# Kernel tuning notes

Measured on AMD Instinct MI355X. Metric: run time of the kernel, lower is better.

The kernel has to match this reference:

```python
import jax, jax.numpy as jnp
import numpy as np
from jax import lax

K = 7          # kernel size
G = 12         # groups
EPS = 1e-5


def bn(x, gamma, beta, axes):
    # training-mode batch norm (torch default train() mode uses batch stats)
    mean = jnp.mean(x, axis=axes, keepdims=True)
    var = jnp.var(x, axis=axes, keepdims=True)
    shape = [1] * x.ndim
    shape[1 if x.ndim == 4 else -1] = -1
    g = gamma.reshape(shape)
    b = beta.reshape(shape)
    return g * (x - mean) * lax.rsqrt(var + EPS) + b


def setup_inputs() -> dict:
    key = jax.random.key(0)
    ks = jax.random.split(key, 12)
    B, C, H, Wd = 16, 192, 32, 32
    Cr = C // 4                      # reduce_mapping out channels = out_channels // reduce_ratio = 48
    flat = C * H * Wd                # 196608
    inp = {
        "x": jax.random.normal(ks[0], (B, C, H, Wd), jnp.float32),
        "Wr": jax.random.normal(ks[1], (Cr, C), jnp.float32) * 0.05,          # reduce_mapping 1x1 conv
        "gamma_s": jnp.ones((Cr,), jnp.float32),
        "beta_s": jnp.zeros((Cr,), jnp.float32),
        "Ws": jax.random.normal(ks[2], (K * K * G, Cr), jnp.float32) * 0.05,  # span_mapping 1x1 conv
        "W1": jax.random.normal(ks[3], (512, flat), jnp.float32) * 0.002,
        "b1": jnp.zeros((512,), jnp.float32),
        "g1": jnp.ones((512,), jnp.float32),
        "beta1": jnp.zeros((512,), jnp.float32),
        "W2": jax.random.normal(ks[4], (128, 512), jnp.float32) * 0.04,
        "b2": jnp.zeros((128,), jnp.float32),
        "g2": jnp.ones((128,), jnp.float32),
        "beta2": jnp.zeros((128,), jnp.float32),
        "W3": jax.random.normal(ks[5], (17, 128), jnp.float32) * 0.09,
        "b3": jnp.zeros((17,), jnp.float32),
    }
    return inp


def reference(x, Wr, gamma_s, beta_s, Ws, W1, b1, g1, beta1, W2, b2, g2, beta2, W3, b3):
    B, C, H, Wd = x.shape
    Cg = C // G
    # unfold (im2col) with kernel 7, pad 3, stride 1, dil 1 -> [B, C*K*K, H, W]
    # channel ordering (c, kh, kw) matches torch.nn.Unfold
    patches = lax.conv_general_dilated_patches(x, (K, K), (1, 1), [(K // 2, K // 2)] * 2)
    unf = patches.reshape(B, G, Cg, K * K, H, Wd)
    # kernel generation path: 1x1 reduce conv -> BN+ReLU -> 1x1 span conv
    red = jnp.einsum('bchw,oc->bohw', x, Wr)
    red = jax.nn.relu(bn(red, gamma_s, beta_s, (0, 2, 3)))
    ker = jnp.einsum('bchw,oc->bohw', red, Ws).reshape(B, G, K * K, H, Wd)
    # involution: per-pixel kernel multiply + sum over K*K
    out = jnp.einsum('bgkhw,bgckhw->bgchw', ker, unf).reshape(B, C, H, Wd)
    # classifier head
    flat = out.reshape(B, -1)
    h = jax.nn.relu(bn(flat @ W1.T + b1, g1, beta1, (0,)))
    h = jax.nn.relu(bn(h @ W2.T + b2, g2, beta2, (0,)))
    return h @ W3.T + b3
```

## Files before the change

### kernel.cpp

```cpp
#include <hip/hip_runtime.h>

#define EPS 1e-5f

typedef float v4f __attribute__((ext_vector_type(4)));

__global__ __launch_bounds__(256) void k_reduce_conv(
    const float* __restrict__ x, const float* __restrict__ Wr,
    float* __restrict__ red, float* __restrict__ spart)
{
  int ob = blockIdx.x >> 6;
  int pb = blockIdx.x & 63;
  int o0 = ob * 6;
  int pix = (pb << 8) + threadIdx.x;
  int b = pix >> 10;
  int hw = pix & 1023;
  const float* xp = x + ((size_t)b * 192) * 1024 + hw;
  float acc[6] = {0.f, 0.f, 0.f, 0.f, 0.f, 0.f};
  for (int c = 0; c < 192; ++c) {
    float xv = xp[(size_t)c * 1024];
#pragma unroll
    for (int j = 0; j < 6; ++j)
      acc[j] = fmaf(xv, Wr[(o0 + j) * 192 + c], acc[j]);
  }
#pragma unroll
  for (int j = 0; j < 6; ++j)
    red[(size_t)(o0 + j) * 16384 + pix] = acc[j];

  int t = threadIdx.x, lane = t & 63, wid = t >> 6;
  float sv[6], qv[6];
#pragma unroll
  for (int j = 0; j < 6; ++j) { sv[j] = acc[j]; qv[j] = acc[j] * acc[j]; }
#pragma unroll
  for (int off = 32; off > 0; off >>= 1)
#pragma unroll
    for (int j = 0; j < 6; ++j) {
      sv[j] += __shfl_down(sv[j], off);
      qv[j] += __shfl_down(qv[j], off);
    }
  __shared__ float ps[4][12];
  if (lane == 0)
#pragma unroll
    for (int j = 0; j < 6; ++j) { ps[wid][j] = sv[j]; ps[wid][6 + j] = qv[j]; }
  __syncthreads();
  if (t < 12) {
    float v = ps[0][t] + ps[1][t] + ps[2][t] + ps[3][t];
    int j = t % 6, s = t / 6;
    spart[(size_t)(s * 48 + o0 + j) * 64 + pb] = v;
  }
}

__global__ __launch_bounds__(128) void k_stats2(
    const float* __restrict__ spart, float* __restrict__ stats)
{
  int t = threadIdx.x;
  if (t < 96) {
    const v4f* p = (const v4f*)(spart + (size_t)t * 64);
    v4f s = p[0];
#pragma unroll
    for (int i = 1; i < 16; ++i) s += p[i];
    stats[t] = s.x + s.y + s.z + s.w;
  }
}

__global__ __launch_bounds__(256) void k_invol(
    const float* __restrict__ x, const float* __restrict__ red,
    const float* __restrict__ stats, const float* __restrict__ gamma_s,
    const float* __restrict__ beta_s, const float* __restrict__ Ws,
    float* __restrict__ flat)
{
  __shared__ __align__(16) float xt[196 * 20];
  __shared__ __align__(16) float redn[64 * 52];
  __shared__ __align__(16) float kt[49 * 64];

  int bx = blockIdx.x;
  int tile = bx & 15;
  int g = (bx >> 4) % 12;
  int b = bx / 192;
  int th = (tile >> 2) * 8, tw = (tile & 3) * 8;
  int t = threadIdx.x;

  for (int idx = t; idx < 16 * 196; idx += 256) {
    int c = idx / 196, s = idx - c * 196;
    int r = s / 14, q = s - r * 14;
    int sh = th + r - 3, sw = tw + q - 3;
    float v = 0.f;
    if (sh >= 0 && sh < 32 && sw >= 0 && sw < 32)
      v = x[(((size_t)b * 192 + g * 16 + c) << 10) + (sh << 5) + sw];
    xt[s * 20 + c] = v;
  }
  for (int idx = t; idx < 64 * 48; idx += 256) {
    int p = idx & 63, o = idx >> 6;
    int py = p >> 3, px = p & 7;
    float mean = stats[o] * (1.f / 16384.f);
    float var = fmaf(-mean, mean, stats[48 + o] * (1.f / 16384.f));
    float sc = gamma_s[o] * rsqrtf(var + EPS);
    float sh_ = fmaf(-mean, sc, beta_s[o]);
    float v = red[(size_t)o * 16384 + (b << 10) + ((th + py) << 5) + (tw + px)];
    redn[p * 52 + o] = fmaxf(fmaf(v, sc, sh_), 0.f);
  }
  __syncthreads();

  {
    int p = t & 63;
    int kg = __builtin_amdgcn_readfirstlane(t >> 6);
    int k0 = kg * 13;
    float acc[13];
#pragma unroll
    for (int j = 0; j < 13; ++j) acc[j] = 0.f;
    const float* wsp = Ws + (size_t)(g * 49 + k0) * 48;
    for (int o4 = 0; o4 < 48; o4 += 4) {
      v4f rv = *(const v4f*)&redn[p * 52 + o4];
#pragma unroll
      for (int j = 0; j < 13; ++j)
        if (k0 + j < 49) {
          acc[j] = fmaf(rv.x, wsp[j * 48 + o4 + 0], acc[j]);
          acc[j] = fmaf(rv.y, wsp[j * 48 + o4 + 1], acc[j]);
          acc[j] = fmaf(rv.z, wsp[j * 48 + o4 + 2], acc[j]);
          acc[j] = fmaf(rv.w, wsp[j * 48 + o4 + 3], acc[j]);
        }
    }
#pragma unroll
    for (int j = 0; j < 13; ++j)
      if (k0 + j < 49) kt[(k0 + j) * 64 + p] = acc[j];
  }
  __syncthreads();

  {
    int p = t & 63, cq = t >> 6;
    int c0 = cq * 4;
    int py = p >> 3, px = p & 7;
    float a0 = 0.f, a1 = 0.f, a2 = 0.f, a3 = 0.f;
#pragma unroll
    for (int k = 0; k < 49; ++k) {
      int dh = k / 7, dw = k - dh * 7;
      float kv = kt[k * 64 + p];
      const v4f xv = *(const v4f*)&xt[((py + dh) * 14 + px + dw) * 20 + c0];
      a0 = fmaf(kv, xv.x, a0);
      a1 = fmaf(kv, xv.y, a1);
      a2 = fmaf(kv, xv.z, a2);
      a3 = fmaf(kv, xv.w, a3);
    }
    size_t base = (((size_t)b * 192 + g * 16 + c0) << 10) + ((th + py) << 5) + (tw + px);
    flat[base] = a0;
    flat[base + 1024] = a1;
    flat[base + 2048] = a2;
    flat[base + 3072] = a3;
  }
}

__global__ __launch_bounds__(256) void k_gemm1(
    const float* __restrict__ flat, const float* __restrict__ W1,
    float* __restrict__ h1part)
{
  int kc = blockIdx.x;
  int n0 = blockIdx.y * 8;
  int t = threadIdx.x;
  int kt = t & 127;
  int bg = t >> 7;
  int b0 = bg * 8;

  const v4f* W1v = (const v4f*)W1;
  const v4f* flatv = (const v4f*)flat;

  float acc[8][8];
#pragma unroll
  for (int n = 0; n < 8; ++n)
#pragma unroll
    for (int j = 0; j < 8; ++j) acc[n][j] = 0.f;

  int kv = kc * 6144 + kt;

  v4f w[8], wn[8], f[8];
#pragma unroll
  for (int n = 0; n < 8; ++n)
    w[n] = W1v[(size_t)(n0 + n) * 49152 + kv];

#define GEMM1_PHASE(CUR, NXT, PRE)                                         \
  {                                                                        \
    _Pragma("unroll")                                                      \
    for (int j = 0; j < 8; ++j)                                            \
      f[j] = flatv[(size_t)(b0 + j) * 49152 + kv];                         \
    if (PRE) {                                                             \
      _Pragma("unroll")                                                    \
      for (int n = 0; n < 8; ++n)                                          \
        NXT[n] = W1v[(size_t)(n0 + n) * 49152 + kv + 128];                 \
    }                                                                      \
    _Pragma("unroll")                                                      \
    for (int j = 0; j < 8; ++j)                                            \
      _Pragma("unroll")                                                    \
      for (int n = 0; n < 8; ++n) {                                        \
        acc[n][j] = fmaf(CUR[n].x, f[j].x, acc[n][j]);                     \
        acc[n][j] = fmaf(CUR[n].y, f[j].y, acc[n][j]);                     \
        acc[n][j] = fmaf(CUR[n].z, f[j].z, acc[n][j]);                     \
        acc[n][j] = fmaf(CUR[n].w, f[j].w, acc[n][j]);                     \
      }                                                                    \
    kv += 128;                                                             \
  }

#pragma unroll 1
  for (int it = 0; it < 24; ++it) {
    GEMM1_PHASE(w, wn, true)
    GEMM1_PHASE(wn, w, (it < 23))
  }
#undef GEMM1_PHASE

  __shared__ float rbuf[256 * 33];
#pragma unroll
  for (int pass = 0; pass < 2; ++pass) {
    __syncthreads();
#pragma unroll
    for (int nn = 0; nn < 4; ++nn)
#pragma unroll
      for (int j = 0; j < 8; ++j)
        rbuf[t * 33 + nn * 8 + j] = acc[pass * 4 + nn][j];
    __syncthreads();
    int v = t >> 2;
    int c = v & 31, bgsel = v >> 5;
    int i = t & 3;
    float s = 0.f;
#pragma unroll
    for (int r = 0; r < 32; ++r)
      s += rbuf[(bgsel * 128 + i + (r << 2)) * 33 + c];
    s += __shfl_down(s, 2, 4);
    s += __shfl_down(s, 1, 4);
    if (i == 0) {
      int nn = c >> 3, j = c & 7;
      int b = bgsel * 8 + j;
      h1part[(size_t)kc * 8192 + b * 512 + n0 + pass * 4 + nn] = s;
    }
  }
}

__global__ __launch_bounds__(256) void k_bn1(
    const float* __restrict__ h1part, const float* __restrict__ g1,
    const float* __restrict__ beta1, float* __restrict__ h1)
{
  int n = blockIdx.x * 256 + threadIdx.x;
  float v[16];
#pragma unroll
  for (int b = 0; b < 16; ++b) v[b] = 0.f;
#pragma unroll
  for (int y = 0; y < 8; ++y)
#pragma unroll
    for (int b = 0; b < 16; ++b)
      v[b] += h1part[(size_t)y * 8192 + b * 512 + n];
  float s = 0.f;
#pragma unroll
  for (int b = 0; b < 16; ++b) s += v[b];
  float mean = s * (1.f / 16.f);
  float q = 0.f;
#pragma unroll
  for (int b = 0; b < 16; ++b) { float d = v[b] - mean; q = fmaf(d, d, q); }
  float inv = rsqrtf(q * (1.f / 16.f) + EPS);
  float sc = g1[n] * inv, sh = beta1[n];
#pragma unroll
  for (int b = 0; b < 16; ++b)
    h1[b * 512 + n] = fmaxf(fmaf(v[b] - mean, sc, sh), 0.f);
}

__global__ __launch_bounds__(256) void k_gemm2(
    const float* __restrict__ h1, const float* __restrict__ W2,
    float* __restrict__ h2pre)
{
  int gid = blockIdx.x * 256 + threadIdx.x;
  int b = gid >> 7, m = gid & 127;
  const float* hp = h1 + b * 512;
  const float* wp = W2 + m * 512;
  float s = 0.f;
  for (int n = 0; n < 512; n += 4) {
    v4f hv = *(const v4f*)(hp + n);
    v4f wv = *(const v4f*)(wp + n);
    s = fmaf(hv.x, wv.x, s);
    s = fmaf(hv.y, wv.y, s);
    s = fmaf(hv.z, wv.z, s);
    s = fmaf(hv.w, wv.w, s);
  }
  h2pre[b * 128 + m] = s;
}

__global__ __launch_bounds__(320) void k_tail(
    const float* __restrict__ h2pre, const float* __restrict__ g2,
    const float* __restrict__ beta2, const float* __restrict__ W3,
    const float* __restrict__ b3, float* __restrict__ out)
{
  __shared__ float h2[16 * 128];
  int t = threadIdx.x;
  if (t < 128) {
    float v[16];
    float s = 0.f;
#pragma unroll
    for (int b = 0; b < 16; ++b) { v[b] = h2pre[b * 128 + t]; s += v[b]; }
    float mean = s * (1.f / 16.f);
    float q = 0.f;
#pragma unroll
    for (int b = 0; b < 16; ++b) { float d = v[b] - mean; q = fmaf(d, d, q); }
    float inv = rsqrtf(q * (1.f / 16.f) + EPS);
    float sc = g2[t] * inv, sh = beta2[t];
#pragma unroll
    for (int b = 0; b < 16; ++b)
      h2[b * 128 + t] = fmaxf(fmaf(v[b] - mean, sc, sh), 0.f);
  }
  __syncthreads();
  if (t < 272) {
    int b = t / 17, j = t - b * 17;
    float s = b3[j];
    const float* hp = h2 + b * 128;
    const float* wp = W3 + j * 128;
#pragma unroll 4
    for (int m = 0; m < 128; ++m) s = fmaf(hp[m], wp[m], s);
    out[t] = s;
  }
}

extern "C" void kernel_launch(void* const* d_in, const int* in_sizes, int n_in,
                              void* d_out, int out_size, void* d_ws, size_t ws_size,
                              hipStream_t stream)
{
  const float* x       = (const float*)d_in[0];
  const float* Wr      = (const float*)d_in[1];
  const float* gamma_s = (const float*)d_in[2];
  const float* beta_s  = (const float*)d_in[3];
  const float* Ws      = (const float*)d_in[4];
  const float* W1      = (const float*)d_in[5];
  const float* g1      = (const float*)d_in[7];
  const float* beta1   = (const float*)d_in[8];
  const float* W2      = (const float*)d_in[9];
  const float* g2      = (const float*)d_in[11];
  const float* beta2   = (const float*)d_in[12];
  const float* W3      = (const float*)d_in[13];
  const float* b3      = (const float*)d_in[14];

  float* ws = (float*)d_ws;
  float* red    = ws;
  float* flat   = red + 786432;
  float* stats  = flat + 3145728;
  float* spart  = stats + 96;
  float* h1part = spart + 6144;
  float* h1     = h1part + 65536;
  float* h2pre  = h1 + 8192;

  k_reduce_conv<<<512, 256, 0, stream>>>(x, Wr, red, spart);
  k_stats2<<<1, 128, 0, stream>>>(spart, stats);
  k_invol<<<3072, 256, 0, stream>>>(x, red, stats, gamma_s, beta_s, Ws, flat);
  k_gemm1<<<dim3(8, 64), 256, 0, stream>>>(flat, W1, h1part);
  k_bn1<<<2, 256, 0, stream>>>(h1part, g1, beta1, h1);
  k_gemm2<<<8, 256, 0, stream>>>(h1, W2, h2pre);
  k_tail<<<1, 320, 0, stream>>>(h2pre, g2, beta2, W3, b3, (float*)d_out);
}
```

Before: 302.3 us.

## Fuse stats into involution, re-tile gemm1, fuse BN1 into gemm2

Removes the single-block stats kernel and has every involution block recompute the BN statistics from the partial sums in shared memory. The big W1 GEMM is re-tiled to 4 outputs per block with half the K-chunk, giving a 16x128 grid (4x more blocks), fewer registers per thread and a launch-bounds occupancy hint. The BN1 kernel is folded into gemm2, so each block redundantly reduces the now-16 partial slices. This cuts two launches and raises parallelism in the dominant GEMM, at the cost of redundant stats work and a larger partial-sum buffer.

```diff
diff --git a/kernel.cpp b/kernel.cpp
--- a/kernel.cpp
+++ b/kernel.cpp
@@ -49,28 +49,16 @@
   }
 }
 
-__global__ __launch_bounds__(128) void k_stats2(
-    const float* __restrict__ spart, float* __restrict__ stats)
-{
-  int t = threadIdx.x;
-  if (t < 96) {
-    const v4f* p = (const v4f*)(spart + (size_t)t * 64);
-    v4f s = p[0];
-#pragma unroll
-    for (int i = 1; i < 16; ++i) s += p[i];
-    stats[t] = s.x + s.y + s.z + s.w;
-  }
-}
-
 __global__ __launch_bounds__(256) void k_invol(
     const float* __restrict__ x, const float* __restrict__ red,
-    const float* __restrict__ stats, const float* __restrict__ gamma_s,
+    const float* __restrict__ spart, const float* __restrict__ gamma_s,
     const float* __restrict__ beta_s, const float* __restrict__ Ws,
     float* __restrict__ flat)
 {
   __shared__ __align__(16) float xt[196 * 20];
   __shared__ __align__(16) float redn[64 * 52];
   __shared__ __align__(16) float kt[49 * 64];
+  __shared__ float sstats[96];
 
   int bx = blockIdx.x;
   int tile = bx & 15;
@@ -78,6 +66,14 @@
   int b = bx / 192;
   int th = (tile >> 2) * 8, tw = (tile & 3) * 8;
   int t = threadIdx.x;
+
+  if (t < 96) {
+    const v4f* p = (const v4f*)(spart + (size_t)t * 64);
+    v4f s4 = p[0];
+#pragma unroll
+    for (int i = 1; i < 16; ++i) s4 += p[i];
+    sstats[t] = s4.x + s4.y + s4.z + s4.w;
+  }
 
   for (int idx = t; idx < 16 * 196; idx += 256) {
     int c = idx / 196, s = idx - c * 196;
@@ -88,11 +84,13 @@
       v = x[(((size_t)b * 192 + g * 16 + c) << 10) + (sh << 5) + sw];
     xt[s * 20 + c] = v;
   }
+  __syncthreads();
+
   for (int idx = t; idx < 64 * 48; idx += 256) {
     int p = idx & 63, o = idx >> 6;
     int py = p >> 3, px = p & 7;
-    float mean = stats[o] * (1.f / 16384.f);
-    float var = fmaf(-mean, mean, stats[48 + o] * (1.f / 16384.f));
+    float mean = sstats[o] * (1.f / 16384.f);
+    float var = fmaf(-mean, mean, sstats[48 + o] * (1.f / 16384.f));
     float sc = gamma_s[o] * rsqrtf(var + EPS);
     float sh_ = fmaf(-mean, sc, beta_s[o]);
     float v = red[(size_t)o * 16384 + (b << 10) + ((th + py) << 5) + (tw + px)];
@@ -148,12 +146,12 @@
   }
 }
 
-__global__ __launch_bounds__(256) void k_gemm1(
+__global__ __launch_bounds__(256, 4) void k_gemm1(
     const float* __restrict__ flat, const float* __restrict__ W1,
     float* __restrict__ h1part)
 {
   int kc = blockIdx.x;
-  int n0 = blockIdx.y * 8;
+  int n0 = blockIdx.y * 4;
   int t = threadIdx.x;
   int kt = t & 127;
   int bg = t >> 7;
@@ -162,17 +160,17 @@
   const v4f* W1v = (const v4f*)W1;
   const v4f* flatv = (const v4f*)flat;
 
-  float acc[8][8];
-#pragma unroll
-  for (int n = 0; n < 8; ++n)
+  float acc[4][8];
+#pragma unroll
+  for (int n = 0; n < 4; ++n)
 #pragma unroll
     for (int j = 0; j < 8; ++j) acc[n][j] = 0.f;
 
-  int kv = kc * 6144 + kt;
-
-  v4f w[8], wn[8], f[8];
-#pragma unroll
-  for (int n = 0; n < 8; ++n)
+  int kv = kc * 3072 + kt;
+
+  v4f w[4], wn[4], f[8];
+#pragma unroll
+  for (int n = 0; n < 4; ++n)
     w[n] = W1v[(size_t)(n0 + n) * 49152 + kv];
 
 #define GEMM1_PHASE(CUR, NXT, PRE)                                         \
@@ -182,13 +180,13 @@
       f[j] = flatv[(size_t)(b0 + j) * 49152 + kv];                         \
     if (PRE) {                                                             \
       _Pragma("unroll")                                                    \
-      for (int n = 0; n < 8; ++n)                                          \
+      for (int n = 0; n < 4; ++n)                                          \
         NXT[n] = W1v[(size_t)(n0 + n) * 49152 + kv + 128];                 \
     }                                                                      \
     _Pragma("unroll")                                                      \
     for (int j = 0; j < 8; ++j)                                            \
       _Pragma("unroll")                                                    \
-      for (int n = 0; n < 8; ++n) {                                        \
+      for (int n = 0; n < 4; ++n) {                                        \
         acc[n][j] = fmaf(CUR[n].x, f[j].x, acc[n][j]);                     \
         acc[n][j] = fmaf(CUR[n].y, f[j].y, acc[n][j]);                     \
         acc[n][j] = fmaf(CUR[n].z, f[j].z, acc[n][j]);                     \
@@ -198,22 +196,20 @@
   }
 
 #pragma unroll 1
-  for (int it = 0; it < 24; ++it) {
+  for (int it = 0; it < 12; ++it) {
     GEMM1_PHASE(w, wn, true)
-    GEMM1_PHASE(wn, w, (it < 23))
+    GEMM1_PHASE(wn, w, (it < 11))
   }
 #undef GEMM1_PHASE
 
   __shared__ float rbuf[256 * 33];
 #pragma unroll
-  for (int pass = 0; pass < 2; ++pass) {
-    __syncthreads();
-#pragma unroll
-    for (int nn = 0; nn < 4; ++nn)
-#pragma unroll
-      for (int j = 0; j < 8; ++j)
-        rbuf[t * 33 + nn * 8 + j] = acc[pass * 4 + nn][j];
-    __syncthreads();
+  for (int nn = 0; nn < 4; ++nn)
+#pragma unroll
+    for (int j = 0; j < 8; ++j)
+      rbuf[t * 33 + nn * 8 + j] = acc[nn][j];
+  __syncthreads();
+  {
     int v = t >> 2;
     int c = v & 31, bgsel = v >> 5;
     int i = t & 3;
@@ -226,56 +222,56 @@
     if (i == 0) {
       int nn = c >> 3, j = c & 7;
       int b = bgsel * 8 + j;
-      h1part[(size_t)kc * 8192 + b * 512 + n0 + pass * 4 + nn] = s;
+      h1part[(size_t)kc * 8192 + b * 512 + n0 + nn] = s;
     }
   }
 }
 
-__global__ __launch_bounds__(256) void k_bn1(
+__global__ __launch_bounds__(256) void k_gemm2(
     const float* __restrict__ h1part, const float* __restrict__ g1,
-    const float* __restrict__ beta1, float* __restrict__ h1)
-{
-  int n = blockIdx.x * 256 + threadIdx.x;
-  float v[16];
-#pragma unroll
-  for (int b = 0; b < 16; ++b) v[b] = 0.f;
-#pragma unroll
-  for (int y = 0; y < 8; ++y)
-#pragma unroll
-    for (int b = 0; b < 16; ++b)
-      v[b] += h1part[(size_t)y * 8192 + b * 512 + n];
-  float s = 0.f;
-#pragma unroll
-  for (int b = 0; b < 16; ++b) s += v[b];
-  float mean = s * (1.f / 16.f);
-  float q = 0.f;
-#pragma unroll
-  for (int b = 0; b < 16; ++b) { float d = v[b] - mean; q = fmaf(d, d, q); }
-  float inv = rsqrtf(q * (1.f / 16.f) + EPS);
-  float sc = g1[n] * inv, sh = beta1[n];
-#pragma unroll
-  for (int b = 0; b < 16; ++b)
-    h1[b * 512 + n] = fmaxf(fmaf(v[b] - mean, sc, sh), 0.f);
-}
-
-__global__ __launch_bounds__(256) void k_gemm2(
-    const float* __restrict__ h1, const float* __restrict__ W2,
+    const float* __restrict__ beta1, const float* __restrict__ W2,
     float* __restrict__ h2pre)
 {
-  int gid = blockIdx.x * 256 + threadIdx.x;
-  int b = gid >> 7, m = gid & 127;
-  const float* hp = h1 + b * 512;
-  const float* wp = W2 + m * 512;
-  float s = 0.f;
-  for (int n = 0; n < 512; n += 4) {
-    v4f hv = *(const v4f*)(hp + n);
-    v4f wv = *(const v4f*)(wp + n);
-    s = fmaf(hv.x, wv.x, s);
-    s = fmaf(hv.y, wv.y, s);
-    s = fmaf(hv.z, wv.z, s);
-    s = fmaf(hv.w, wv.w, s);
-  }
-  h2pre[b * 128 + m] = s;
+  __shared__ __align__(16) float h1s[2][512];
+  int t = threadIdx.x;
+  int b0 = blockIdx.x * 2;
+
+#pragma unroll
+  for (int rep = 0; rep < 2; ++rep) {
+    int n = rep * 256 + t;
+    float v[16];
+#pragma unroll
+    for (int b = 0; b < 16; ++b) v[b] = 0.f;
+    for (int y = 0; y < 16; ++y)
+#pragma unroll
+      for (int b = 0; b < 16; ++b)
+        v[b] += h1part[(size_t)y * 8192 + b * 512 + n];
+    float s = 0.f;
+#pragma unroll
+    for (int b = 0; b < 16; ++b) s += v[b];
+    float mean = s * (1.f / 16.f);
+    float q = 0.f;
+#pragma unroll
+    for (int b = 0; b < 16; ++b) { float d = v[b] - mean; q = fmaf(d, d, q); }
+    float inv = rsqrtf(q * (1.f / 16.f) + EPS);
+    float sc = g1[n] * inv, sh = beta1[n];
+    h1s[0][n] = fmaxf(fmaf(v[b0] - mean, sc, sh), 0.f);
+    h1s[1][n] = fmaxf(fmaf(v[b0 + 1] - mean, sc, sh), 0.f);
+  }
+  __syncthreads();
+
+  int m = t & 127, bsel = t >> 7;
+  const v4f* W2v = (const v4f*)W2;
+  v4f sa = {0.f, 0.f, 0.f, 0.f};
+  for (int nv = 0; nv < 128; ++nv) {
+    v4f wv = W2v[(size_t)m * 128 + nv];
+    v4f hv = *(const v4f*)&h1s[bsel][nv * 4];
+    sa.x = fmaf(hv.x, wv.x, sa.x);
+    sa.y = fmaf(hv.y, wv.y, sa.y);
+    sa.z = fmaf(hv.z, wv.z, sa.z);
+    sa.w = fmaf(hv.w, wv.w, sa.w);
+  }
+  h2pre[(b0 + bsel) * 128 + m] = (sa.x + sa.y) + (sa.z + sa.w);
 }
 
 __global__ __launch_bounds__(320) void k_tail(
@@ -333,17 +329,13 @@
   float* ws = (float*)d_ws;
   float* red    = ws;
   float* flat   = red + 786432;
-  float* stats  = flat + 3145728;
-  float* spart  = stats + 96;
+  float* spart  = flat + 3145728;
   float* h1part = spart + 6144;
-  float* h1     = h1part + 65536;
-  float* h2pre  = h1 + 8192;
+  float* h2pre  = h1part + 131072;
 
   k_reduce_conv<<<512, 256, 0, stream>>>(x, Wr, red, spart);
-  k_stats2<<<1, 128, 0, stream>>>(spart, stats);
-  k_invol<<<3072, 256, 0, stream>>>(x, red, stats, gamma_s, beta_s, Ws, flat);
-  k_gemm1<<<dim3(8, 64), 256, 0, stream>>>(flat, W1, h1part);
-  k_bn1<<<2, 256, 0, stream>>>(h1part, g1, beta1, h1);
-  k_gemm2<<<8, 256, 0, stream>>>(h1, W2, h2pre);
+  k_invol<<<3072, 256, 0, stream>>>(x, red, spart, gamma_s, beta_s, Ws, flat);
+  k_gemm1<<<dim3(16, 128), 256, 0, stream>>>(flat, W1, h1part);
+  k_gemm2<<<8, 256, 0, stream>>>(h1part, g1, beta1, W2, h2pre);
   k_tail<<<1, 320, 0, stream>>>(h2pre, g2, beta2, W3, b3, (float*)d_out);
 }
```

Measured after the change: 578.6 us. +91.4%, slower.
